# Kernel tuning notes

Hardware: AMD Instinct MI355X
Metric: run time of the kernel (lower is better)

## Reference

```python
import jax, jax.numpy as jnp
import numpy as np

N = 131072   # number of points
C = 128      # channels
H = 8        # heads
D = C // H   # head dim = 16
K = 48       # patch (window) size
P = 3000     # number of path segments


def _build_indices():
    """Faithful numpy replica of PathAttention.get_padding_and_inverse (index-only, no_grad)."""
    rng = np.random.default_rng(0)
    lengths = rng.integers(K + 1, 3 * K, size=P)          # all > K -> padded to multiple of K
    M = int(lengths.sum())
    bpad = ((lengths + K - 1) // K) * K
    off = np.concatenate([[0], np.cumsum(lengths)])
    offp = np.concatenate([[0], np.cumsum(bpad)])
    Mpad = int(offp[-1])
    pad = np.arange(Mpad)
    unpad = np.arange(M)
    for i in range(P):
        o0, o1, p0, p1 = off[i], off[i + 1], offp[i], offp[i + 1]
        unpad[o0:o1] += p0 - o0
        b = int(lengths[i])
        if b != bpad[i]:
            r = b % K
            # replicate previous window's tail into the padded region
            pad[p1 - K + r:p1] = pad[p1 - 2 * K + r:p1 - K]
        pad[p0:p1] -= p0 - o0
    # every point appears at least once so the scatter-mean covers all N rows
    inv = np.concatenate([rng.permutation(N), rng.integers(0, N, M - N)])
    rng.shuffle(inv)
    return pad, unpad, inv


def setup_inputs() -> dict:
    pad, unpad, inv = _build_indices()
    M = unpad.shape[0]
    key = jax.random.key(0)
    ks = jax.random.split(key, 8)
    s = 0.02
    theta = jax.random.uniform(ks[1], (M, D), minval=0.0, maxval=2.0 * np.pi)
    return {
        "feat": jax.random.normal(ks[0], (N, C), jnp.float32),
        "cos": jnp.cos(theta).astype(jnp.float32),
        "sin": jnp.sin(theta).astype(jnp.float32),
        "g1": jnp.ones((C,), jnp.float32),
        "b1": jnp.zeros((C,), jnp.float32),
        "qkv_w": (jax.random.normal(ks[2], (3 * C, C)) * s).astype(jnp.float32),
        "qkv_b": jnp.zeros((3 * C,), jnp.float32),
        "proj_w": (jax.random.normal(ks[3], (C, C)) * s).astype(jnp.float32),
        "proj_b": jnp.zeros((C,), jnp.float32),
        "g2": jnp.ones((C,), jnp.float32),
        "b2": jnp.zeros((C,), jnp.float32),
        "fc1_w": (jax.random.normal(ks[4], (4 * C, C)) * s).astype(jnp.float32),
        "fc1_b": jnp.zeros((4 * C,), jnp.float32),
        "fc2_w": (jax.random.normal(ks[5], (C, 4 * C)) * s).astype(jnp.float32),
        "fc2_b": jnp.zeros((C,), jnp.float32),
        "path_inverse": jnp.asarray(inv, jnp.int32),
        "pad": jnp.asarray(pad, jnp.int32),
        "unpad": jnp.asarray(unpad, jnp.int32),
        "num_heads": H,
        "patch_size": K,
    }


def _ln(x, g, b):
    m = x.mean(-1, keepdims=True)
    v = x.var(-1, keepdims=True)
    return (x - m) / jnp.sqrt(v + 1e-5) * g + b


def reference(feat, cos, sin, g1, b1, qkv_w, qkv_b, proj_w, proj_b, g2, b2,
              fc1_w, fc1_b, fc2_w, fc2_b, path_inverse, pad, unpad,
              num_heads, patch_size):
    Np, Cc = feat.shape
    Hh = num_heads
    Dd = Cc // Hh
    Kk = patch_size
    # pre-norm + qkv projection, then path gather and pad gather
    h = _ln(feat, g1, b1)
    qkv = (h @ qkv_w.T + qkv_b)[path_inverse][pad]          # [Mpad, 3C]
    Mpad = qkv.shape[0]
    qkv = qkv.reshape(Mpad, 3, Hh, Dd)
    q, k, v = qkv[:, 0], qkv[:, 1], qkv[:, 2]               # [Mpad, H, D]
    # non-interleaved rope (flash-attn apply_rotary_emb with cos of dim D//2)
    cp = cos[pad][:, :Dd // 2][:, None, :]                  # [Mpad, 1, D/2]
    sp = sin[pad][:, :Dd // 2][:, None, :]
    def rope(x):
        x1, x2 = x[..., :Dd // 2], x[..., Dd // 2:]
        return jnp.concatenate([x1 * cp - x2 * sp, x2 * cp + x1 * sp], axis=-1)
    q = rope(q)
    k = rope(k)
    # windowed attention: all windows are exactly K after padding
    Wn = Mpad // Kk
    qw = q.reshape(Wn, Kk, Hh, Dd)
    kw = k.reshape(Wn, Kk, Hh, Dd)
    vw = v.reshape(Wn, Kk, Hh, Dd)
    scores = jnp.einsum('wqhd,wkhd->whqk', qw, kw) * (Dd ** -0.5)
    p = jax.nn.softmax(scores, axis=-1)
    o = jnp.einsum('whqk,wkhd->wqhd', p, vw).reshape(Mpad, Cc)
    # unpad gather, output projection, scatter-mean combine over overlapping paths
    o = o[unpad] @ proj_w.T + proj_b                        # [M, C]
    sums = jax.ops.segment_sum(o, path_inverse, num_segments=Np)
    cnt = jax.ops.segment_sum(jnp.ones((o.shape[0],), o.dtype), path_inverse, num_segments=Np)
    a = sums / jnp.maximum(cnt, 1.0)[:, None]
    x = feat + a
    # MLP branch
    h2 = _ln(x, g2, b2)
    m = jax.nn.gelu(h2 @ fc1_w.T + fc1_b, approximate=False) @ fc2_w.T + fc2_b
    return x + m
```

## Files before the change

kernel.cpp:

```cpp
#include <hip/hip_runtime.h>


typedef __attribute__((ext_vector_type(4))) float f32x4;
typedef __attribute__((ext_vector_type(8))) short bf16x8;
typedef __attribute__((ext_vector_type(4))) short bf16x4;
typedef __attribute__((ext_vector_type(2))) unsigned u32x2;

#define MFMA(a, b, c) __builtin_amdgcn_mfma_f32_16x16x32_bf16(a, b, c, 0, 0, 0)

static __device__ __forceinline__ short f2bf(float x) {
  union { float f; unsigned u; } v; v.f = x;
  unsigned r = v.u + 0x7FFFu + ((v.u >> 16) & 1u);
  return (short)(r >> 16);
}
static __device__ __forceinline__ float bf2f(short b) {
  union { unsigned u; float f; } v;
  v.u = ((unsigned)(unsigned short)b) << 16;
  return v.f;
}
static __device__ __forceinline__ unsigned cvt_pk_bf16(float lo, float hi) {
  unsigned r;
  asm("v_cvt_pk_bf16_f32 %0, %1, %2" : "=v"(r) : "v"(lo), "v"(hi));
  return r;
}
static __device__ __forceinline__ float exp2_f(float x) {
  float r; asm("v_exp_f32 %0, %1" : "=v"(r) : "v"(x)); return r;
}
static __device__ __forceinline__ void gload_lds16(const void* g, void* l) {
  __builtin_amdgcn_global_load_lds(
      (const __attribute__((address_space(1))) void*)g,
      (__attribute__((address_space(3))) void*)l, 16, 0, 0);
}

static __device__ __forceinline__ float gelu_f(float v) {
  float e = exp2_f(v * -2.4554669f);
  return v * __builtin_amdgcn_rcpf(1.0f + e);
}

__global__ void k_cvt(const float* __restrict__ s, short* __restrict__ d, int n) {
  int i = blockIdx.x * 256 + threadIdx.x;
  if (i < n) d[i] = f2bf(s[i]);
}

__global__ void k_pack_w1(const float* __restrict__ w, short* __restrict__ d) {
  int i = blockIdx.x * 256 + threadIdx.x;
  int j = i & 7;  int r = i >> 3;
  int g = r & 3;  r >>= 2;
  int u = r & 15; r >>= 4;
  int kk = r & 3; int t = r >> 2;
  d[i] = f2bf(w[(t * 16 + u) * 128 + kk * 32 + g * 8 + j]);
}

__global__ void k_pack_b1(const float* __restrict__ b, float* __restrict__ d) {
  int i = blockIdx.x * 256 + threadIdx.x;
  if (i < 512) {
    int reg = i & 3; int r = i >> 2;
    int g = r & 3;   int t = r >> 2;
    d[i] = b[16 * t + 4 * g + reg];
  }
}

__global__ void k_cnt(const int* __restrict__ pinv, int* __restrict__ cnt, int M) {
  int i = blockIdx.x * 256 + threadIdx.x;
  if (i < M) atomicAdd(&cnt[pinv[i]], 1);
}

__global__ __launch_bounds__(256) void k_scan1(const int* __restrict__ cnt,
                                               int* __restrict__ lpre,
                                               int* __restrict__ bsum) {
  const int i = blockIdx.x * 256 + threadIdx.x;
  const int t = threadIdx.x, lane = t & 63, wid = t >> 6;
  int v = cnt[i];
  int x = v;
#pragma unroll
  for (int d = 1; d < 64; d <<= 1) {
    int y = __shfl_up(x, d);
    if (lane >= d) x += y;
  }
  __shared__ int wsum[4];
  if (lane == 63) wsum[wid] = x;
  __syncthreads();
  int add = 0;
#pragma unroll
  for (int wv = 0; wv < 4; wv++) add += (wv < wid) ? wsum[wv] : 0;
  lpre[i] = x + add - v;
  if (t == 255) bsum[blockIdx.x] = x + add;
}

__global__ __launch_bounds__(512) void k_scan2(int* __restrict__ bsum, int nb) {
  const int t = threadIdx.x, lane = t & 63, wid = t >> 6;
  int v = (t < nb) ? bsum[t] : 0;
  int x = v;
#pragma unroll
  for (int d = 1; d < 64; d <<= 1) {
    int y = __shfl_up(x, d);
    if (lane >= d) x += y;
  }
  __shared__ int wsum[8];
  if (lane == 63) wsum[wid] = x;
  __syncthreads();
  int add = 0;
#pragma unroll
  for (int wv = 0; wv < 8; wv++) add += (wv < wid) ? wsum[wv] : 0;
  if (t < nb) bsum[t] = x + add - v;
}

__global__ void k_place(const int* __restrict__ pinv, const int* __restrict__ lpre,
                        const int* __restrict__ bsum, int* __restrict__ cursor,
                        int* __restrict__ idxl, int M) {
  int m = blockIdx.x * 256 + threadIdx.x;
  if (m < M) {
    int n = pinv[m];
    int slot = atomicAdd(&cursor[n], 1);
    idxl[lpre[n] + bsum[n >> 8] + slot] = m;
  }
}

__global__ __launch_bounds__(256) void k1_ln_qkv(
    const float* __restrict__ feat, const float* __restrict__ g1,
    const float* __restrict__ b1, const short* __restrict__ wq,
    const float* __restrict__ bq, short* __restrict__ qkvb) {
  __shared__ short h_lds[32 * 128];
  __shared__ short o_st[32 * 384];
  const int blk = blockIdx.x, t = threadIdx.x;
  {
    const int r = t >> 3, oct = t & 7;
    const float* fp = feat + (size_t)(blk * 32 + r) * 128 + oct * 16;
    float vals[16];
    float s = 0.f, s2 = 0.f;
#pragma unroll
    for (int i = 0; i < 4; i++) {
      f32x4 v = *(const f32x4*)(fp + i * 4);
#pragma unroll
      for (int j = 0; j < 4; j++) { float x = v[j]; vals[i * 4 + j] = x; s += x; s2 += x * x; }
    }
    s += __shfl_xor(s, 1);  s += __shfl_xor(s, 2);  s += __shfl_xor(s, 4);
    s2 += __shfl_xor(s2, 1); s2 += __shfl_xor(s2, 2); s2 += __shfl_xor(s2, 4);
    float mean = s * (1.f / 128.f);
    float rstd = rsqrtf(s2 * (1.f / 128.f) - mean * mean + 1e-5f);
    const int sw = (r & 7) << 4;
#pragma unroll
    for (int gi = 0; gi < 2; gi++) {
      bf16x8 wv;
#pragma unroll
      for (int j = 0; j < 8; j++) {
        int c = oct * 16 + gi * 8 + j;
        wv[j] = f2bf((vals[gi * 8 + j] - mean) * rstd * g1[c] + b1[c]);
      }
      *(bf16x8*)((char*)h_lds + r * 256 + ((oct * 32 + gi * 16) ^ sw)) = wv;
    }
  }
  __syncthreads();
  const int wave = t >> 6, lane = t & 63, u = lane & 15, g = lane >> 4;
  f32x4 acc[2][6];
  f32x4 zz = {0.f, 0.f, 0.f, 0.f};
#pragma unroll
  for (int a = 0; a < 2; a++)
#pragma unroll
    for (int b = 0; b < 6; b++) acc[a][b] = zz;
#pragma unroll
  for (int kk = 0; kk < 4; kk++) {
    bf16x8 af[2];
#pragma unroll
    for (int rt = 0; rt < 2; rt++)
      af[rt] = *(const bf16x8*)((char*)h_lds + (rt * 16 + u) * 256 +
                                ((kk * 64 + g * 16) ^ ((u & 7) << 4)));
    bf16x8 bfr[6];
#pragma unroll
    for (int ct = 0; ct < 6; ct++) {
      int col = wave * 96 + ct * 16 + u;
      bfr[ct] = *(const bf16x8*)(wq + (size_t)col * 128 + kk * 32 + g * 8);
    }
#pragma unroll
    for (int rt = 0; rt < 2; rt++)
#pragma unroll
      for (int ct = 0; ct < 6; ct++) acc[rt][ct] = MFMA(af[rt], bfr[ct], acc[rt][ct]);
  }
#pragma unroll
  for (int rt = 0; rt < 2; rt++)
#pragma unroll
    for (int ct = 0; ct < 6; ct++) {
      int col = wave * 96 + ct * 16 + u;
      float bias = bq[col];
#pragma unroll
      for (int reg = 0; reg < 4; reg++) {
        int rowl = rt * 16 + 4 * g + reg;
        *(short*)((char*)o_st + rowl * 768 + ((col * 2) ^ (g << 5))) =
            f2bf(acc[rt][ct][reg] + bias);
      }
    }
  __syncthreads();
  for (int idx = t; idx < 1536; idx += 256) {
    int r = idx / 48, c8 = idx % 48;
    bf16x8 v = *(const bf16x8*)((char*)o_st + r * 768 +
                                ((c8 * 16) ^ ((((r >> 2) & 3)) << 5)));
    *(bf16x8*)(qkvb + ((size_t)blk * 32 + r) * 384 + c8 * 8) = v;
  }
}

__global__ __launch_bounds__(512) void k2_attn(
    const short* __restrict__ qkv, const float* __restrict__ cosb,
    const float* __restrict__ sinb, const int* __restrict__ pinv,
    const int* __restrict__ padv, const int* __restrict__ unpadv,
    short* __restrict__ ocmp) {
  __shared__ short qo_lds[48 * 136];
  __shared__ short k_lds[48 * 128];
  __shared__ short vT[8 * 16 * 64];
  __shared__ int midx_s[48];
  __shared__ int gidx_s[48];
  __shared__ int canon_s[48];
  __shared__ float cs_s[48 * 8];
  __shared__ float sn_s[48 * 8];

  const int w = blockIdx.x;
  const int t = threadIdx.x;

  if (t < 48) {
    int pp = w * 48 + t;
    int m = padv[pp];
    midx_s[t] = m;
    gidx_s[t] = pinv[m];
    canon_s[t] = (unpadv[m] == pp) ? 1 : 0;
    const float* cp = cosb + (size_t)m * 16;
    const float* sp = sinb + (size_t)m * 16;
#pragma unroll
    for (int i = 0; i < 2; i++) {
      *(f32x4*)(cs_s + t * 8 + i * 4) = *(const f32x4*)(cp + i * 4);
      *(f32x4*)(sn_s + t * 8 + i * 4) = *(const f32x4*)(sp + i * 4);
    }
  }
  __syncthreads();

  {
    const int r = t >> 3, seg = t & 7;
    if (r < 48) {
      const short* rowp = qkv + (size_t)gidx_s[r] * 384;
      const float* cpr = cs_s + r * 8;
      const float* spr = sn_s + r * 8;
#pragma unroll
      for (int ci = 0; ci < 3; ci++) {
        const int c0 = seg * 48 + ci * 16;
        const int sec = c0 >> 7;
        const int hh = (c0 & 127) >> 4;
        bf16x8 lo = *(const bf16x8*)(rowp + c0);
        bf16x8 hi = *(const bf16x8*)(rowp + c0 + 8);
        if (sec < 2) {
          union { unsigned d[4]; bf16x8 v; } w0, w1;
#pragma unroll
          for (int j2 = 0; j2 < 4; j2++) {
            float x1a = bf2f(lo[2 * j2]),     x1b = bf2f(lo[2 * j2 + 1]);
            float x2a = bf2f(hi[2 * j2]),     x2b = bf2f(hi[2 * j2 + 1]);
            float ca = cpr[2 * j2], cb = cpr[2 * j2 + 1];
            float sa = spr[2 * j2], sb = spr[2 * j2 + 1];
            w0.d[j2] = cvt_pk_bf16(x1a * ca - x2a * sa, x1b * cb - x2b * sb);
            w1.d[j2] = cvt_pk_bf16(fmaf(x2a, ca, x1a * sa), fmaf(x2b, cb, x1b * sb));
          }
          char* dst = (char*)(sec == 0 ? qo_lds : k_lds);
          int sw = (r & 7) << 4;
          *(bf16x8*)(dst + r * 256 + ((hh * 32) ^ sw)) = w0.v;
          *(bf16x8*)(dst + r * 256 + ((hh * 32 + 16) ^ sw)) = w1.v;
        } else {
          const int hsw = (hh & 7) << 4;
#pragma unroll
          for (int d = 0; d < 16; d++) {
            short val = (d < 8) ? lo[d] : hi[d - 8];
            *(short*)((char*)vT + hh * 2048 + d * 128 +
                      ((r * 2) ^ ((d & 15) << 3) ^ hsw)) = val;
          }
        }
      }
    } else {
#pragma unroll
      for (int ci = 0; ci < 3; ci++) {
        const int c0 = seg * 48 + ci * 16;
        if (c0 >= 256) {
          const int hh = (c0 & 127) >> 4;
          const int hsw = (hh & 7) << 4;
#pragma unroll
          for (int d = 0; d < 16; d++)
            *(short*)((char*)vT + hh * 2048 + d * 128 +
                      ((r * 2) ^ ((d & 15) << 3) ^ hsw)) = 0;
        }
      }
    }
  }
  __syncthreads();

  const int h = t >> 6, lane = t & 63, u = lane & 15, g = lane >> 4;
  const int sbase = h * 32 + g * 16;
  bf16x8 zf = {0, 0, 0, 0, 0, 0, 0, 0};
  bf16x8 kf[3], qf[3];
#pragma unroll
  for (int i = 0; i < 3; i++) {
    int kj = i * 16 + u;
    if (g < 2) {
      kf[i] = *(const bf16x8*)((char*)k_lds + kj * 256 + (sbase ^ ((kj & 7) << 4)));
      qf[i] = *(const bf16x8*)((char*)qo_lds + kj * 256 + (sbase ^ ((kj & 7) << 4)));
    } else { kf[i] = zf; qf[i] = zf; }
  }
  union UU { bf16x8 v8; bf16x4 v4[2]; unsigned d[4]; };
  UU a1, a2;
  {
    const int dbase = h * 2048 + u * 128;
    const int sw = ((u & 15) << 3) ^ ((h & 7) << 4);
    a1.v4[0] = *(const bf16x4*)((char*)vT + dbase + ((8 * g) ^ sw));
    a1.v4[1] = *(const bf16x4*)((char*)vT + dbase + ((32 + 8 * g) ^ sw));
    a2.v4[0] = *(const bf16x4*)((char*)vT + dbase + ((64 + 8 * g) ^ sw));
    a2.v4[1] = *(const bf16x4*)((char*)vT + dbase + ((96 + 8 * g) ^ sw));
  }
  __syncthreads();

  f32x4 d1[3][3];
#pragma unroll
  for (int a = 0; a < 3; a++)
#pragma unroll
    for (int b = 0; b < 3; b++) {
      f32x4 z = {0.f, 0.f, 0.f, 0.f};
      d1[a][b] = MFMA(kf[a], qf[b], z);
    }

  const float C = 0.36067376022224085f;
  float rl[3];
#pragma unroll
  for (int qt = 0; qt < 3; qt++) {
    float sm = 0.f;
#pragma unroll
    for (int kt = 0; kt < 3; kt++)
#pragma unroll
      for (int rr = 0; rr < 4; rr++) {
        float e = exp2_f(d1[kt][qt][rr] * C);
        d1[kt][qt][rr] = e;
        sm += e;
      }
    sm += __shfl_xor(sm, 16);
    sm += __shfl_xor(sm, 32);
    rl[qt] = __builtin_amdgcn_rcpf(sm);
  }

#pragma unroll
  for (int qt = 0; qt < 3; qt++) {
    UU bu1, bu2;
    bu1.d[0] = cvt_pk_bf16(d1[0][qt][0], d1[0][qt][1]);
    bu1.d[1] = cvt_pk_bf16(d1[0][qt][2], d1[0][qt][3]);
    bu1.d[2] = cvt_pk_bf16(d1[1][qt][0], d1[1][qt][1]);
    bu1.d[3] = cvt_pk_bf16(d1[1][qt][2], d1[1][qt][3]);
    bu2.d[0] = cvt_pk_bf16(d1[2][qt][0], d1[2][qt][1]);
    bu2.d[1] = cvt_pk_bf16(d1[2][qt][2], d1[2][qt][3]);
    bu2.d[2] = 0; bu2.d[3] = 0;
    f32x4 z = {0.f, 0.f, 0.f, 0.f};
    f32x4 acc = MFMA(a1.v8, bu1.v8, z);
    acc = MFMA(a2.v8, bu2.v8, acc);
    const float rq = rl[qt];
    u32x2 ov;
    ov[0] = cvt_pk_bf16(acc[0] * rq, acc[1] * rq);
    ov[1] = cvt_pk_bf16(acc[2] * rq, acc[3] * rq);
    *(u32x2*)((char*)qo_lds + (qt * 16 + u) * 272 + h * 32 + g * 8) = ov;
  }
  __syncthreads();
  for (int idx = t; idx < 768; idx += 512) {
    int r = idx >> 4, c8 = idx & 15;
    if (canon_s[r]) {
      *(bf16x8*)(ocmp + (size_t)midx_s[r] * 128 + c8 * 8) =
          *(const bf16x8*)((char*)qo_lds + r * 272 + c8 * 16);
    }
  }
}

__global__ __launch_bounds__(256) void k3_proj(
    const short* __restrict__ ocmp, const short* __restrict__ wp,
    const float* __restrict__ pb, short* __restrict__ oproj, int M) {
  __shared__ short o_st[64 * 128];
  const int blk = blockIdx.x, t = threadIdx.x;
  const int m0 = blk * 64;
  const int wave = t >> 6, lane = t & 63, u = lane & 15, g = lane >> 4;
  f32x4 acc[4][2];
  f32x4 zz = {0.f, 0.f, 0.f, 0.f};
#pragma unroll
  for (int a = 0; a < 4; a++) { acc[a][0] = zz; acc[a][1] = zz; }
  bf16x8 zf = {0, 0, 0, 0, 0, 0, 0, 0};
#pragma unroll
  for (int kk = 0; kk < 4; kk++) {
    bf16x8 af[4];
#pragma unroll
    for (int rt = 0; rt < 4; rt++) {
      int m = m0 + rt * 16 + u;
      af[rt] = (m < M) ? *(const bf16x8*)(ocmp + (size_t)m * 128 + kk * 32 + g * 8) : zf;
    }
    bf16x8 bfr[2];
#pragma unroll
    for (int ct = 0; ct < 2; ct++) {
      int col = wave * 32 + ct * 16 + u;
      bfr[ct] = *(const bf16x8*)(wp + (size_t)col * 128 + kk * 32 + g * 8);
    }
#pragma unroll
    for (int rt = 0; rt < 4; rt++)
#pragma unroll
      for (int ct = 0; ct < 2; ct++) acc[rt][ct] = MFMA(af[rt], bfr[ct], acc[rt][ct]);
  }
#pragma unroll
  for (int rt = 0; rt < 4; rt++)
#pragma unroll
    for (int ct = 0; ct < 2; ct++) {
      int col = wave * 32 + ct * 16 + u;
      float bias = pb[col];
#pragma unroll
      for (int reg = 0; reg < 4; reg++) {
        int rowl = rt * 16 + 4 * g + reg;
        *(short*)((char*)o_st + rowl * 256 + ((col * 2) ^ (g << 5))) =
            f2bf(acc[rt][ct][reg] + bias);
      }
    }
  __syncthreads();
#pragma unroll
  for (int it = 0; it < 4; it++) {
    int idx = t + it * 256;
    int r = idx >> 4, c8 = idx & 15;
    if (m0 + r < M) {
      bf16x8 v = *(const bf16x8*)((char*)o_st + r * 256 +
                                  ((c8 * 16) ^ (((r >> 2) & 3) << 5)));
      *(bf16x8*)(oproj + (size_t)(m0 + r) * 128 + c8 * 8) = v;
    }
  }
}

__global__ __launch_bounds__(256) void k4a_gather_ln(
    const float* __restrict__ feat, float* __restrict__ dout,
    const int* __restrict__ cnt, const int* __restrict__ lpre,
    const int* __restrict__ bsum, const int* __restrict__ idxl,
    const short* __restrict__ oproj,
    const float* __restrict__ g2, const float* __restrict__ b2,
    short* __restrict__ hbuf) {
  const int t = threadIdx.x;
  const int r = t >> 3, oct = t & 7;
  const int n = blockIdx.x * 32 + r;
  const int c = cnt[n];
  const int start = lpre[n] + bsum[n >> 8];
  float sum[16];
#pragma unroll
  for (int i = 0; i < 16; i++) sum[i] = 0.f;
  for (int j = 0; j < c; j++) {
    int m = idxl[start + j];
    const short* op = oproj + (size_t)m * 128 + oct * 16;
    bf16x8 v0 = *(const bf16x8*)op;
    bf16x8 v1 = *(const bf16x8*)(op + 8);
#pragma unroll
    for (int q = 0; q < 8; q++) { sum[q] += bf2f(v0[q]); sum[8 + q] += bf2f(v1[q]); }
  }
  const float rc = 1.0f / fmaxf((float)c, 1.0f);
  const float* fp = feat + (size_t)n * 128 + oct * 16;
  float* xp = dout + (size_t)n * 128 + oct * 16;
  float vals[16];
  float s = 0.f, s2 = 0.f;
#pragma unroll
  for (int i = 0; i < 4; i++) {
    f32x4 fv = *(const f32x4*)(fp + i * 4);
    f32x4 xv;
#pragma unroll
    for (int j = 0; j < 4; j++) {
      float x = fv[j] + sum[i * 4 + j] * rc;
      xv[j] = x; vals[i * 4 + j] = x; s += x; s2 += x * x;
    }
    *(f32x4*)(xp + i * 4) = xv;
  }
  s += __shfl_xor(s, 1);  s += __shfl_xor(s, 2);  s += __shfl_xor(s, 4);
  s2 += __shfl_xor(s2, 1); s2 += __shfl_xor(s2, 2); s2 += __shfl_xor(s2, 4);
  float mean = s * (1.f / 128.f);
  float rstd = rsqrtf(s2 * (1.f / 128.f) - mean * mean + 1e-5f);
  bf16x8 h0, h1;
#pragma unroll
  for (int j = 0; j < 8; j++) {
    int c0 = oct * 16 + j, c1 = oct * 16 + 8 + j;
    h0[j] = f2bf((vals[j] - mean) * rstd * g2[c0] + b2[c0]);
    h1[j] = f2bf((vals[8 + j] - mean) * rstd * g2[c1] + b2[c1]);
  }
  short* hp = hbuf + (size_t)n * 128 + oct * 16;
  *(bf16x8*)hp = h0;
  *(bf16x8*)(hp + 8) = h1;
}

__global__ __launch_bounds__(256) void k4b1_fc1(
    const short* __restrict__ hbuf, const short* __restrict__ w1p,
    const float* __restrict__ b1p, short* __restrict__ p0,
    short* __restrict__ p1, int R0) {
  __shared__ __align__(16) char wbuf[2][16384];
  const int blk = blockIdx.x, t = threadIdx.x;
  const int wave = t >> 6, lane = t & 63, u = lane & 15, g = lane >> 4;
  const int row0 = blk * 64 + wave * 16;
  const int row = row0 + u;

  bf16x8 hf[4];
#pragma unroll
  for (int kk = 0; kk < 4; kk++)
    hf[kk] = *(const bf16x8*)(hbuf + (size_t)row * 128 + kk * 32 + g * 8);

  short* dstrow = (row0 < R0) ? (p0 + (size_t)row * 512)
                              : (p1 + ((size_t)(row - R0)) * 512);

  auto stage = [&](int b, int tg) {
#pragma unroll
    for (int it = 0; it < 4; it++) {
      const short* gp = w1p + (size_t)tg * 8192 + (it * 4 + wave) * 512 + lane * 8;
      gload_lds16(gp, &wbuf[b][(it * 4 + wave) * 1024]);
    }
  };

  const int frag_off = (u * 4 + g) * 16;
  stage(0, 0);
#pragma unroll
  for (int tg = 0; tg < 8; tg++) {
    const int b = tg & 1;
    if (tg < 7) stage(b ^ 1, tg + 1);
    __syncthreads();
#pragma unroll
    for (int tl = 0; tl < 4; tl++) {
      const int tt = tg * 4 + tl;
      f32x4 acc = *(const f32x4*)(b1p + (tt * 4 + g) * 4);
#pragma unroll
      for (int kk = 0; kk < 4; kk++) {
        bf16x8 w1f = *(const bf16x8*)(&wbuf[b][(tl * 4 + kk) * 1024 + frag_off]);
        acc = MFMA(w1f, hf[kk], acc);
      }
      u32x2 pv;
      pv[0] = cvt_pk_bf16(gelu_f(acc[0]), gelu_f(acc[1]));
      pv[1] = cvt_pk_bf16(gelu_f(acc[2]), gelu_f(acc[3]));
      *(u32x2*)(dstrow + tt * 16 + g * 4) = pv;
    }
    __syncthreads();
  }
}

__global__ __launch_bounds__(256) void k4b2_fc2(
    const short* __restrict__ p0, const short* __restrict__ p1, int R0,
    const short* __restrict__ w2, const float* __restrict__ bb2,
    float* __restrict__ dout) {
  __shared__ __align__(16) char tile[2][16384];
  const int blk = blockIdx.x, t = threadIdx.x;
  const int row0 = blk * 64;
  const short* pb_ = (row0 < R0) ? (p0 + (size_t)row0 * 512)
                                 : (p1 + (size_t)(row0 - R0) * 512);
  const int wave = t >> 6, lane = t & 63, u = lane & 15, g = lane >> 4;

  auto stage = [&](int b, int ks) {
#pragma unroll
    for (int it = 0; it < 4; it++) {
      int ci = (it * 4 + wave) * 64 + lane;
      int r = ci >> 4, c = ci & 15;
      const short* gp = pb_ + (size_t)r * 512 + ks * 128 + ((c ^ (r & 7)) * 8);
      gload_lds16(gp, &tile[b][(it * 4 + wave) * 1024]);
    }
  };

  f32x4 acc[4][2];
  f32x4 zz = {0.f, 0.f, 0.f, 0.f};
#pragma unroll
  for (int a = 0; a < 4; a++) { acc[a][0] = zz; acc[a][1] = zz; }

  stage(0, 0);
#pragma unroll
  for (int ks = 0; ks < 4; ks++) {
    const int b = ks & 1;
    bf16x8 bfr[4][2];
#pragma unroll
    for (int kk = 0; kk < 4; kk++)
#pragma unroll
      for (int ct = 0; ct < 2; ct++)
        bfr[kk][ct] = *(const bf16x8*)(w2 + (size_t)(wave * 32 + ct * 16 + u) * 512 +
                                       ks * 128 + kk * 32 + g * 8);
    if (ks < 3) stage(b ^ 1, ks + 1);
    __syncthreads();
#pragma unroll
    for (int kk = 0; kk < 4; kk++) {
      bf16x8 af[4];
#pragma unroll
      for (int rt = 0; rt < 4; rt++)
        af[rt] = *(const bf16x8*)(&tile[b][(rt * 16 + u) * 256 +
                                           (((kk * 4 + g) ^ (u & 7)) * 16)]);
#pragma unroll
      for (int rt = 0; rt < 4; rt++)
#pragma unroll
        for (int ct = 0; ct < 2; ct++)
          acc[rt][ct] = MFMA(af[rt], bfr[kk][ct], acc[rt][ct]);
    }
    __syncthreads();
  }

#pragma unroll
  for (int rt = 0; rt < 4; rt++)
#pragma unroll
    for (int ct = 0; ct < 2; ct++) {
      int col = wave * 32 + ct * 16 + u;
      float bias = bb2[col];
#pragma unroll
      for (int reg = 0; reg < 4; reg++) {
        size_t rr = (size_t)row0 + rt * 16 + 4 * g + reg;
        float* p = dout + rr * 128 + col;
        *p = *p + acc[rt][ct][reg] + bias;
      }
    }
}

extern "C" void kernel_launch(void* const* d_in, const int* in_sizes, int n_in,
                              void* d_out, int out_size, void* d_ws, size_t ws_size,
                              hipStream_t stream) {
  (void)n_in; (void)out_size; (void)ws_size;
  const float* feat   = (const float*)d_in[0];
  const float* cosb   = (const float*)d_in[1];
  const float* sinb   = (const float*)d_in[2];
  const float* g1     = (const float*)d_in[3];
  const float* b1     = (const float*)d_in[4];
  const float* qkv_w  = (const float*)d_in[5];
  const float* qkv_b  = (const float*)d_in[6];
  const float* proj_w = (const float*)d_in[7];
  const float* proj_b = (const float*)d_in[8];
  const float* g2     = (const float*)d_in[9];
  const float* b2     = (const float*)d_in[10];
  const float* fc1_w  = (const float*)d_in[11];
  const float* fc1_b  = (const float*)d_in[12];
  const float* fc2_w  = (const float*)d_in[13];
  const float* fc2_b  = (const float*)d_in[14];
  const int* pinv     = (const int*)d_in[15];
  const int* padv     = (const int*)d_in[16];
  const int* unpadv   = (const int*)d_in[17];

  const int N    = in_sizes[0] / 128;
  const int M    = in_sizes[15];
  const int Mpad = in_sizes[16];
  const int Wn   = Mpad / 48;
  const int R0   = (N / 4) * 3;

  float* dout = (float*)d_out;
  char* ws = (char*)d_ws;

  size_t szQ = (size_t)N * 384 * 2;
  size_t szO = (size_t)M * 128 * 2;

  short* qkvb  = (short*)ws;
  short* oproj = (short*)ws;
  short* p0    = (short*)ws;
  short* ocmp  = (short*)(ws + szQ);
  short* hbuf  = (short*)(ws + szQ);
  short* p1    = (short*)(ws + szQ + (size_t)N * 256);

  size_t offI = ((size_t)M * 256 + 255) & ~(size_t)255;
  int* cnt    = (int*)(ws + offI);
  int* cursor = cnt + N;
  int* lpre   = cursor + N;
  int* bsum   = lpre + N;
  int* idxl   = bsum + 1024;

  size_t offW = szQ + szO;
  short* wq_b = (short*)(ws + offW);
  short* wp_b = wq_b + 49152;
  short* w1p  = wp_b + 16384;
  short* w2_b = w1p + 65536;
  float* b1p  = (float*)(w2_b + 65536);

  k_cvt<<<(49152 + 255) / 256, 256, 0, stream>>>(qkv_w, wq_b, 49152);
  k_cvt<<<(16384 + 255) / 256, 256, 0, stream>>>(proj_w, wp_b, 16384);
  k_pack_w1<<<256, 256, 0, stream>>>(fc1_w, w1p);
  k_cvt<<<(65536 + 255) / 256, 256, 0, stream>>>(fc2_w, w2_b, 65536);
  k_pack_b1<<<2, 256, 0, stream>>>(fc1_b, b1p);

  k1_ln_qkv<<<N / 32, 256, 0, stream>>>(feat, g1, b1, wq_b, qkv_b, qkvb);
  k2_attn<<<Wn, 512, 0, stream>>>(qkvb, cosb, sinb, pinv, padv, unpadv, ocmp);

  hipMemsetAsync(cnt, 0, (size_t)N * 4, stream);
  hipMemsetAsync(cursor, 0, (size_t)N * 4, stream);
  k_cnt<<<(M + 255) / 256, 256, 0, stream>>>(pinv, cnt, M);
  k_scan1<<<N / 256, 256, 0, stream>>>(cnt, lpre, bsum);
  k_scan2<<<1, 512, 0, stream>>>(bsum, N / 256);
  k_place<<<(M + 255) / 256, 256, 0, stream>>>(pinv, lpre, bsum, cursor, idxl, M);

  k3_proj<<<(M + 63) / 64, 256, 0, stream>>>(ocmp, wp_b, proj_b, oproj, M);
  k4a_gather_ln<<<N / 32, 256, 0, stream>>>(feat, dout, cnt, lpre, bsum, idxl,
                                            oproj, g2, b2, hbuf);
  k4b1_fc1<<<N / 64, 256, 0, stream>>>(hbuf, w1p, b1p, p0, p1, R0);
  k4b2_fc2<<<N / 64, 256, 0, stream>>>(p0, p1, R0, w2_b, fc2_b, dout);
}
```

Measured before the change: 446.3 us.

## Stage packed weights in LDS and write GEMM outputs directly in QKV/proj kernels

Weight prep is merged into a single kernel that packs qkv_w and proj_w into an MFMA-fragment layout, along with the biases. k1 now handles 64 rows per block. It double-buffers the packed QKV weights into LDS with global_load_lds and swaps MFMA operands so each lane writes its output row directly, dropping the LDS output staging. k3 loads all proj weights into LDS once and also writes straight to global. The intent is to cut the redundant per-wave global weight loads, the staging round-trips and the launch overhead. The cost is more LDS use per block and lower occupancy.

After: 418.3 us. 1.07x faster.

```diff
diff --git a/kernel.cpp b/kernel.cpp
--- a/kernel.cpp
+++ b/kernel.cpp
@@ -37,27 +37,39 @@
   return v * __builtin_amdgcn_rcpf(1.0f + e);
 }
 
-__global__ void k_cvt(const float* __restrict__ s, short* __restrict__ d, int n) {
-  int i = blockIdx.x * 256 + threadIdx.x;
-  if (i < n) d[i] = f2bf(s[i]);
-}
-
-__global__ void k_pack_w1(const float* __restrict__ w, short* __restrict__ d) {
-  int i = blockIdx.x * 256 + threadIdx.x;
+static __device__ __forceinline__ void pack_w(const float* __restrict__ w,
+                                              short* __restrict__ d, int i) {
   int j = i & 7;  int r = i >> 3;
   int g = r & 3;  r >>= 2;
   int u = r & 15; r >>= 4;
   int kk = r & 3; int t = r >> 2;
   d[i] = f2bf(w[(t * 16 + u) * 128 + kk * 32 + g * 8 + j]);
 }
-
-__global__ void k_pack_b1(const float* __restrict__ b, float* __restrict__ d) {
+static __device__ __forceinline__ void pack_b(const float* __restrict__ b,
+                                              float* __restrict__ d, int i) {
+  int reg = i & 3; int r = i >> 2;
+  int g = r & 3;   int t = r >> 2;
+  d[i] = b[16 * t + 4 * g + reg];
+}
+__global__ void k_prep(const float* __restrict__ qkv_w,
+                       const float* __restrict__ proj_w,
+                       const float* __restrict__ fc1_w,
+                       const float* __restrict__ fc2_w,
+                       const float* __restrict__ qkv_b,
+                       const float* __restrict__ fc1_b,
+                       const float* __restrict__ proj_b,
+                       short* __restrict__ wqp, short* __restrict__ wpp,
+                       short* __restrict__ w1p, short* __restrict__ w2b,
+                       float* __restrict__ bqp, float* __restrict__ b1p,
+                       float* __restrict__ pbp) {
   int i = blockIdx.x * 256 + threadIdx.x;
-  if (i < 512) {
-    int reg = i & 3; int r = i >> 2;
-    int g = r & 3;   int t = r >> 2;
-    d[i] = b[16 * t + 4 * g + reg];
-  }
+  if (i < 49152)        pack_w(qkv_w, wqp, i);
+  else if (i < 65536)   pack_w(proj_w, wpp, i - 49152);
+  else if (i < 131072)  pack_w(fc1_w, w1p, i - 65536);
+  else if (i < 196608)  w2b[i - 131072] = f2bf(fc2_w[i - 131072]);
+  else if (i < 197120)  pack_b(fc1_b, b1p, i - 196608);
+  else if (i < 197504)  pack_b(qkv_b, bqp, i - 197120);
+  else if (i < 197632)  pack_b(proj_b, pbp, i - 197504);
 }
 
 __global__ void k_cnt(const int* __restrict__ pinv, int* __restrict__ cnt, int M) {
@@ -118,83 +130,83 @@
 
 __global__ __launch_bounds__(256) void k1_ln_qkv(
     const float* __restrict__ feat, const float* __restrict__ g1,
-    const float* __restrict__ b1, const short* __restrict__ wq,
-    const float* __restrict__ bq, short* __restrict__ qkvb) {
-  __shared__ short h_lds[32 * 128];
-  __shared__ short o_st[32 * 384];
+    const float* __restrict__ b1, const short* __restrict__ wqp,
+    const float* __restrict__ bqp, short* __restrict__ qkvb) {
+  __shared__ short h_lds[64 * 128];
+  __shared__ __align__(16) char wbuf[2][16384];
   const int blk = blockIdx.x, t = threadIdx.x;
+  const int wave = t >> 6, lane = t & 63, u = lane & 15, g = lane >> 4;
+
   {
-    const int r = t >> 3, oct = t & 7;
-    const float* fp = feat + (size_t)(blk * 32 + r) * 128 + oct * 16;
-    float vals[16];
+    const int r = t >> 2, quad = t & 3;
+    const float* fp = feat + (size_t)(blk * 64 + r) * 128 + quad * 32;
+    float vals[32];
     float s = 0.f, s2 = 0.f;
 #pragma unroll
-    for (int i = 0; i < 4; i++) {
+    for (int i = 0; i < 8; i++) {
       f32x4 v = *(const f32x4*)(fp + i * 4);
 #pragma unroll
       for (int j = 0; j < 4; j++) { float x = v[j]; vals[i * 4 + j] = x; s += x; s2 += x * x; }
     }
-    s += __shfl_xor(s, 1);  s += __shfl_xor(s, 2);  s += __shfl_xor(s, 4);
-    s2 += __shfl_xor(s2, 1); s2 += __shfl_xor(s2, 2); s2 += __shfl_xor(s2, 4);
+    s += __shfl_xor(s, 1);  s += __shfl_xor(s, 2);
+    s2 += __shfl_xor(s2, 1); s2 += __shfl_xor(s2, 2);
     float mean = s * (1.f / 128.f);
     float rstd = rsqrtf(s2 * (1.f / 128.f) - mean * mean + 1e-5f);
     const int sw = (r & 7) << 4;
 #pragma unroll
-    for (int gi = 0; gi < 2; gi++) {
+    for (int gi = 0; gi < 4; gi++) {
       bf16x8 wv;
 #pragma unroll
       for (int j = 0; j < 8; j++) {
-        int c = oct * 16 + gi * 8 + j;
+        int c = quad * 32 + gi * 8 + j;
         wv[j] = f2bf((vals[gi * 8 + j] - mean) * rstd * g1[c] + b1[c]);
       }
-      *(bf16x8*)((char*)h_lds + r * 256 + ((oct * 32 + gi * 16) ^ sw)) = wv;
-    }
-  }
-  __syncthreads();
-  const int wave = t >> 6, lane = t & 63, u = lane & 15, g = lane >> 4;
-  f32x4 acc[2][6];
-  f32x4 zz = {0.f, 0.f, 0.f, 0.f};
-#pragma unroll
-  for (int a = 0; a < 2; a++)
-#pragma unroll
-    for (int b = 0; b < 6; b++) acc[a][b] = zz;
-#pragma unroll
-  for (int kk = 0; kk < 4; kk++) {
-    bf16x8 af[2];
-#pragma unroll
-    for (int rt = 0; rt < 2; rt++)
-      af[rt] = *(const bf16x8*)((char*)h_lds + (rt * 16 + u) * 256 +
-                                ((kk * 64 + g * 16) ^ ((u & 7) << 4)));
-    bf16x8 bfr[6];
-#pragma unroll
-    for (int ct = 0; ct < 6; ct++) {
-      int col = wave * 96 + ct * 16 + u;
-      bfr[ct] = *(const bf16x8*)(wq + (size_t)col * 128 + kk * 32 + g * 8);
-    }
-#pragma unroll
-    for (int rt = 0; rt < 2; rt++)
-#pragma unroll
-      for (int ct = 0; ct < 6; ct++) acc[rt][ct] = MFMA(af[rt], bfr[ct], acc[rt][ct]);
-  }
-#pragma unroll
-  for (int rt = 0; rt < 2; rt++)
-#pragma unroll
-    for (int ct = 0; ct < 6; ct++) {
-      int col = wave * 96 + ct * 16 + u;
-      float bias = bq[col];
-#pragma unroll
-      for (int reg = 0; reg < 4; reg++) {
-        int rowl = rt * 16 + 4 * g + reg;
-        *(short*)((char*)o_st + rowl * 768 + ((col * 2) ^ (g << 5))) =
-            f2bf(acc[rt][ct][reg] + bias);
+      *(bf16x8*)((char*)h_lds + r * 256 + ((quad * 64 + gi * 16) ^ sw)) = wv;
+    }
+  }
+
+  auto stage = [&](int b, int tg) {
+#pragma unroll
+    for (int it = 0; it < 4; it++) {
+      const short* gp = wqp + (size_t)tg * 8192 + (it * 4 + wave) * 512 + lane * 8;
+      gload_lds16(gp, &wbuf[b][(it * 4 + wave) * 1024]);
+    }
+  };
+
+  stage(0, 0);
+  __syncthreads();
+
+  bf16x8 hf[4];
+  const int hrow = wave * 16 + u;
+#pragma unroll
+  for (int kk = 0; kk < 4; kk++)
+    hf[kk] = *(const bf16x8*)((char*)h_lds + hrow * 256 +
+                              ((kk * 64 + g * 16) ^ ((u & 7) << 4)));
+
+  const int row = blk * 64 + hrow;
+  short* dstrow = qkvb + (size_t)row * 384;
+  const int frag_off = (u * 4 + g) * 16;
+
+#pragma unroll
+  for (int tg = 0; tg < 6; tg++) {
+    const int b = tg & 1;
+    if (tg < 5) stage(b ^ 1, tg + 1);
+    if (tg > 0) __syncthreads();
+#pragma unroll
+    for (int tl = 0; tl < 4; tl++) {
+      const int tt = tg * 4 + tl;
+      f32x4 acc = *(const f32x4*)(bqp + (tt * 4 + g) * 4);
+#pragma unroll
+      for (int kk = 0; kk < 4; kk++) {
+        bf16x8 wf = *(const bf16x8*)(&wbuf[b][(tl * 4 + kk) * 1024 + frag_off]);
+        acc = MFMA(wf, hf[kk], acc);
       }
-    }
-  __syncthreads();
-  for (int idx = t; idx < 1536; idx += 256) {
-    int r = idx / 48, c8 = idx % 48;
-    bf16x8 v = *(const bf16x8*)((char*)o_st + r * 768 +
-                                ((c8 * 16) ^ ((((r >> 2) & 3)) << 5)));
-    *(bf16x8*)(qkvb + ((size_t)blk * 32 + r) * 384 + c8 * 8) = v;
+      u32x2 pv;
+      pv[0] = cvt_pk_bf16(acc[0], acc[1]);
+      pv[1] = cvt_pk_bf16(acc[2], acc[3]);
+      *(u32x2*)(dstrow + tt * 16 + g * 4) = pv;
+    }
+    __syncthreads();
   }
 }
 
@@ -367,58 +379,41 @@
 }
 
 __global__ __launch_bounds__(256) void k3_proj(
-    const short* __restrict__ ocmp, const short* __restrict__ wp,
-    const float* __restrict__ pb, short* __restrict__ oproj, int M) {
-  __shared__ short o_st[64 * 128];
+    const short* __restrict__ ocmp, const short* __restrict__ wpp,
+    const float* __restrict__ pbp, short* __restrict__ oproj, int M) {
+  __shared__ __align__(16) char wbuf[32768];
   const int blk = blockIdx.x, t = threadIdx.x;
-  const int m0 = blk * 64;
   const int wave = t >> 6, lane = t & 63, u = lane & 15, g = lane >> 4;
-  f32x4 acc[4][2];
-  f32x4 zz = {0.f, 0.f, 0.f, 0.f};
-#pragma unroll
-  for (int a = 0; a < 4; a++) { acc[a][0] = zz; acc[a][1] = zz; }
-  bf16x8 zf = {0, 0, 0, 0, 0, 0, 0, 0};
-#pragma unroll
-  for (int kk = 0; kk < 4; kk++) {
-    bf16x8 af[4];
-#pragma unroll
-    for (int rt = 0; rt < 4; rt++) {
-      int m = m0 + rt * 16 + u;
-      af[rt] = (m < M) ? *(const bf16x8*)(ocmp + (size_t)m * 128 + kk * 32 + g * 8) : zf;
-    }
-    bf16x8 bfr[2];
-#pragma unroll
-    for (int ct = 0; ct < 2; ct++) {
-      int col = wave * 32 + ct * 16 + u;
-      bfr[ct] = *(const bf16x8*)(wp + (size_t)col * 128 + kk * 32 + g * 8);
-    }
-#pragma unroll
-    for (int rt = 0; rt < 4; rt++)
-#pragma unroll
-      for (int ct = 0; ct < 2; ct++) acc[rt][ct] = MFMA(af[rt], bfr[ct], acc[rt][ct]);
-  }
-#pragma unroll
-  for (int rt = 0; rt < 4; rt++)
-#pragma unroll
-    for (int ct = 0; ct < 2; ct++) {
-      int col = wave * 32 + ct * 16 + u;
-      float bias = pb[col];
-#pragma unroll
-      for (int reg = 0; reg < 4; reg++) {
-        int rowl = rt * 16 + 4 * g + reg;
-        *(short*)((char*)o_st + rowl * 256 + ((col * 2) ^ (g << 5))) =
-            f2bf(acc[rt][ct][reg] + bias);
-      }
-    }
-  __syncthreads();
-#pragma unroll
-  for (int it = 0; it < 4; it++) {
-    int idx = t + it * 256;
-    int r = idx >> 4, c8 = idx & 15;
-    if (m0 + r < M) {
-      bf16x8 v = *(const bf16x8*)((char*)o_st + r * 256 +
-                                  ((c8 * 16) ^ (((r >> 2) & 3) << 5)));
-      *(bf16x8*)(oproj + (size_t)(m0 + r) * 128 + c8 * 8) = v;
+  const int row = blk * 64 + wave * 16 + u;
+
+#pragma unroll
+  for (int it = 0; it < 8; it++) {
+    const int c = it * 4 + wave;
+    gload_lds16(wpp + (size_t)c * 512 + lane * 8, &wbuf[c * 1024]);
+  }
+
+  bf16x8 of[4];
+#pragma unroll
+  for (int kk = 0; kk < 4; kk++)
+    of[kk] = *(const bf16x8*)(ocmp + (size_t)row * 128 + kk * 32 + g * 8);
+
+  __syncthreads();
+
+  const int frag_off = (u * 4 + g) * 16;
+  short* dstrow = oproj + (size_t)row * 128;
+#pragma unroll
+  for (int tt = 0; tt < 8; tt++) {
+    f32x4 acc = *(const f32x4*)(pbp + (tt * 4 + g) * 4);
+#pragma unroll
+    for (int kk = 0; kk < 4; kk++) {
+      bf16x8 wf = *(const bf16x8*)(&wbuf[(tt * 4 + kk) * 1024 + frag_off]);
+      acc = MFMA(wf, of[kk], acc);
+    }
+    if (row < M) {
+      u32x2 pv;
+      pv[0] = cvt_pk_bf16(acc[0], acc[1]);
+      pv[1] = cvt_pk_bf16(acc[2], acc[3]);
+      *(u32x2*)(dstrow + tt * 16 + g * 4) = pv;
     }
   }
 }
@@ -649,19 +644,19 @@
   int* idxl   = bsum + 1024;
 
   size_t offW = szQ + szO;
-  short* wq_b = (short*)(ws + offW);
-  short* wp_b = wq_b + 49152;
-  short* w1p  = wp_b + 16384;
+  short* wqp  = (short*)(ws + offW);
+  short* wpp  = wqp + 49152;
+  short* w1p  = wpp + 16384;
   short* w2_b = w1p + 65536;
   float* b1p  = (float*)(w2_b + 65536);
-
-  k_cvt<<<(49152 + 255) / 256, 256, 0, stream>>>(qkv_w, wq_b, 49152);
-  k_cvt<<<(16384 + 255) / 256, 256, 0, stream>>>(proj_w, wp_b, 16384);
-  k_pack_w1<<<256, 256, 0, stream>>>(fc1_w, w1p);
-  k_cvt<<<(65536 + 255) / 256, 256, 0, stream>>>(fc2_w, w2_b, 65536);
-  k_pack_b1<<<2, 256, 0, stream>>>(fc1_b, b1p);
-
-  k1_ln_qkv<<<N / 32, 256, 0, stream>>>(feat, g1, b1, wq_b, qkv_b, qkvb);
+  float* bqp  = b1p + 512;
+  float* pbp  = bqp + 384;
+
+  k_prep<<<772, 256, 0, stream>>>(qkv_w, proj_w, fc1_w, fc2_w,
+                                  qkv_b, fc1_b, proj_b,
+                                  wqp, wpp, w1p, w2_b, bqp, b1p, pbp);
+
+  k1_ln_qkv<<<N / 64, 256, 0, stream>>>(feat, g1, b1, wqp, bqp, qkvb);
   k2_attn<<<Wn, 512, 0, stream>>>(qkvb, cosb, sinb, pinv, padv, unpadv, ocmp);
 
   hipMemsetAsync(cnt, 0, (size_t)N * 4, stream);
@@ -671,7 +666,7 @@
   k_scan2<<<1, 512, 0, stream>>>(bsum, N / 256);
   k_place<<<(M + 255) / 256, 256, 0, stream>>>(pinv, lpre, bsum, cursor, idxl, M);
 
-  k3_proj<<<(M + 63) / 64, 256, 0, stream>>>(ocmp, wp_b, proj_b, oproj, M);
+  k3_proj<<<(M + 63) / 64, 256, 0, stream>>>(ocmp, wpp, pbp, oproj, M);
   k4a_gather_ln<<<N / 32, 256, 0, stream>>>(feat, dout, cnt, lpre, bsum, idxl,
                                             oproj, g2, b2, hbuf);
   k4b1_fc1<<<N / 64, 256, 0, stream>>>(hbuf, w1p, b1p, p0, p1, R0);
```
